# Performance work log

Hardware: AMD Instinct MI355X
Metric: run time of the kernel (lower is better)

## Reference

```python
import jax, jax.numpy as jnp
import numpy as np

NUM_LAYERS = 4
HIDDEN = 64
IN_CH = 3
OUT_CH = 1


def setup_inputs() -> dict:
    key = jax.random.key(0)
    ks = jax.random.split(key, 16)
    s = 0.1  # weight init scale
    x = jax.random.normal(ks[0], (2, 64, 64, IN_CH), dtype=jnp.float32)
    lift_w = jax.random.normal(ks[1], (IN_CH, HIDDEN), dtype=jnp.float32) * s
    lift_b = jax.random.normal(ks[2], (HIDDEN,), dtype=jnp.float32) * s
    blk_w = jax.random.normal(ks[3], (NUM_LAYERS, HIDDEN, HIDDEN), dtype=jnp.float32) * s
    blk_b = jax.random.normal(ks[4], (NUM_LAYERS, HIDDEN), dtype=jnp.float32) * s
    q_w = jax.random.normal(ks[5], (NUM_LAYERS, HIDDEN, HIDDEN), dtype=jnp.float32) * s
    q_b = jax.random.normal(ks[6], (NUM_LAYERS, HIDDEN), dtype=jnp.float32) * s
    k_w = jax.random.normal(ks[7], (NUM_LAYERS, HIDDEN, HIDDEN), dtype=jnp.float32) * s
    k_b = jax.random.normal(ks[8], (NUM_LAYERS, HIDDEN), dtype=jnp.float32) * s
    v_w = jax.random.normal(ks[9], (NUM_LAYERS, HIDDEN, HIDDEN), dtype=jnp.float32) * s
    v_b = jax.random.normal(ks[10], (NUM_LAYERS, HIDDEN), dtype=jnp.float32) * s
    proj_w = jax.random.normal(ks[11], (HIDDEN, OUT_CH), dtype=jnp.float32) * s
    proj_b = jax.random.normal(ks[12], (OUT_CH,), dtype=jnp.float32) * s
    return {"x": x, "lift_w": lift_w, "lift_b": lift_b,
            "blk_w": blk_w, "blk_b": blk_b,
            "q_w": q_w, "q_b": q_b, "k_w": k_w, "k_b": k_b,
            "v_w": v_w, "v_b": v_b, "proj_w": proj_w, "proj_b": proj_b}


def reference(x, lift_w, lift_b, blk_w, blk_b, q_w, q_b, k_w, k_b, v_w, v_b, proj_w, proj_b):
    prefix = x.shape[:-1]           # (B, H, W)
    B = x.shape[0]
    xf = x.reshape(B, -1, x.shape[-1])   # [B, N, in_ch]
    N = xf.shape[1]
    h = xf @ lift_w + lift_b             # [B, N, d]
    d = h.shape[-1]
    scale = 1.0 / jnp.sqrt(jnp.float32(d))
    for i in range(NUM_LAYERS):
        q = h @ q_w[i] + q_b[i]
        k = h @ k_w[i] + k_b[i]
        v = h @ v_w[i] + v_b[i]
        # full dense kernel, as in torch.bmm(q, k^T)/sqrt(d)
        kern = jnp.einsum('bnd,bmd->bnm', q, k) * scale     # [B, N, N]
        integral = jnp.einsum('bnm,bmd->bnd', kern, v) / N  # [B, N, d]
        wh = h @ blk_w[i] + blk_b[i]
        h = jax.nn.gelu(wh + integral, approximate=False)   # torch F.gelu default = exact erf
    out = h @ proj_w + proj_b                               # [B, N, out_ch]
    return out.reshape(*prefix, out.shape[-1])
```

## Files before the change

kernel.cpp:

```cpp
#include <hip/hip_runtime.h>
#include <hip/hip_bf16.h>
#include <math.h>


#define NLAYER 4
#define NB 2
#define NN 4096
#define DD 64
#define RPB 32
#define NT 256
#define NBLK 256
#define SHP 68
#define C0F (1.0f/32768.0f)
#define PSZ 2304
#define NCH 128
#define CHW 18

typedef __hip_bfloat16 bf16;
typedef unsigned long long u64t;

__device__ __forceinline__ float b2f(const bf16 v) { return __bfloat162float(v); }

template <typename T> struct Acc;
template <> struct Acc<float> {
    static __device__ __forceinline__ float ld(const void* p, int i) { return ((const float*)p)[i]; }
    static __device__ __forceinline__ void st(void* p, int i, float v) { ((float*)p)[i] = v; }
};
template <> struct Acc<bf16> {
    static __device__ __forceinline__ float ld(const void* p, int i) { return b2f(((const bf16*)p)[i]); }
    static __device__ __forceinline__ void st(void* p, int i, float v) { ((bf16*)p)[i] = __float2bfloat16(v); }
};

__device__ __forceinline__ float gelu_exact(float x) {
    return 0.5f * x * (1.0f + erff(x * 0.70710678118654752f));
}

__device__ __forceinline__ float2 ldc2(const float* p) {
    u64t v = __hip_atomic_load((const u64t*)p, __ATOMIC_RELAXED, __HIP_MEMORY_SCOPE_AGENT);
    float2 r;
    r.x = __uint_as_float((unsigned)v);
    r.y = __uint_as_float((unsigned)(v >> 32));
    return r;
}
__device__ __forceinline__ void stc2(float* p, float a, float b) {
    u64t v = ((u64t)__float_as_uint(b) << 32) | (u64t)__float_as_uint(a);
    __hip_atomic_store((u64t*)p, v, __ATOMIC_RELAXED, __HIP_MEMORY_SCOPE_AGENT);
}
__device__ __forceinline__ unsigned ldw(unsigned* p) {
    return __hip_atomic_load(p, __ATOMIC_RELAXED, __HIP_MEMORY_SCOPE_AGENT);
}
__device__ __forceinline__ void stw(unsigned* p, unsigned v) {
    __hip_atomic_store(p, v, __ATOMIC_RELAXED, __HIP_MEMORY_SCOPE_AGENT);
}
__device__ __forceinline__ void pollw(unsigned* p, unsigned ep) {
    int guard = 0;
    while (ldw(p) < ep && ++guard < (1 << 18)) __builtin_amdgcn_s_sleep(2);
}

__device__ __forceinline__ void mm4x4(float (&acc)[4][4],
    float4 L0, float4 L1, float4 L2, float4 L3,
    float4 R0, float4 R1, float4 R2, float4 R3)
{
    const float L[4][4] = {{L0.x,L0.y,L0.z,L0.w},{L1.x,L1.y,L1.z,L1.w},
                           {L2.x,L2.y,L2.z,L2.w},{L3.x,L3.y,L3.z,L3.w}};
    const float R[4][4] = {{R0.x,R0.y,R0.z,R0.w},{R1.x,R1.y,R1.z,R1.w},
                           {R2.x,R2.y,R2.z,R2.w},{R3.x,R3.y,R3.z,R3.w}};
    #pragma unroll
    for (int a = 0; a < 4; a++)
        #pragma unroll
        for (int k = 0; k < 4; k++)
            #pragma unroll
            for (int b = 0; b < 4; b++)
                acc[a][b] += L[a][k] * R[k][b];
}

__device__ __forceinline__ void mmNT4x4(float (&acc)[4][4],
    float4 L0, float4 L1, float4 L2, float4 L3,
    float4 R0, float4 R1, float4 R2, float4 R3)
{
    const float L[4][4] = {{L0.x,L0.y,L0.z,L0.w},{L1.x,L1.y,L1.z,L1.w},
                           {L2.x,L2.y,L2.z,L2.w},{L3.x,L3.y,L3.z,L3.w}};
    const float R[4][4] = {{R0.x,R0.y,R0.z,R0.w},{R1.x,R1.y,R1.z,R1.w},
                           {R2.x,R2.y,R2.z,R2.w},{R3.x,R3.y,R3.z,R3.w}};
    #pragma unroll
    for (int a = 0; a < 4; a++)
        #pragma unroll
        for (int b = 0; b < 4; b++)
            #pragma unroll
            for (int k = 0; k < 4; k++)
                acc[a][b] += L[a][k] * R[b][k];
}

__device__ __forceinline__ void outer4x4(float (&acc)[4][4], float4 A, float4 B)
{
    const float Aa[4] = {A.x, A.y, A.z, A.w};
    const float Ba[4] = {B.x, B.y, B.z, B.w};
    #pragma unroll
    for (int a = 0; a < 4; a++)
        #pragma unroll
        for (int b = 0; b < 4; b++)
            acc[a][b] += Aa[a] * Ba[b];
}


#define SM_SS   23936
#define SM_SU   24000
#define SM_BK   24064
#define SM_BQ   24128
#define SM_BV   24192
#define SM_BE   24256
#define SM_QK   24320
#define SM_KQ   24384
#define SM_QBK  24448
#define SM_RED  24512
#define SM_TOT  24768

template <typename T>
__device__ void run_net(
    const void* x, const void* lw, const void* lb,
    const void* blkw, const void* blkb,
    const void* qw, const void* qb, const void* kw, const void* kb,
    const void* vw, const void* vb, const void* pw, const void* pb,
    void* out, float* Gpart, float* Gg,
    unsigned* aflag, unsigned* cflag,
    float* smem, int blk, int t)
{
    float (*sH)[SHP] = (float(*)[SHP])(smem);
    float (*B1)[SHP] = (float(*)[SHP])(smem + 2176);
    float (*B2)[SHP] = (float(*)[SHP])(smem + 6528);
    float (*B3)[SHP] = (float(*)[SHP])(smem + 10880);
    float (*B4)[SHP] = (float(*)[SHP])(smem + 15232);
    float (*B5)[SHP] = (float(*)[SHP])(smem + 19584);
    float* PS  = smem + 10880;
    float* RED = smem + 10880;
    float* sS  = smem + SM_SS;
    float* suS = smem + SM_SU;
    float* bkS = smem + SM_BK;
    float* bqS = smem + SM_BQ;
    float* bvS = smem + SM_BV;
    float* beS = smem + SM_BE;
    float* qkS = smem + SM_QK;
    float* kqS = smem + SM_KQ;
    float* qbkS = smem + SM_QBK;
    float (*red)[DD] = (float(*)[DD])(smem + SM_RED);

    const int row0 = blk * RPB;
    const int bb = blk >> 7;
    const int r = t >> 4, c4 = (t & 15) << 2;
    const int i4 = t >> 4, j4 = t & 15;
    const int r0 = i4 << 2, c0 = j4 << 2;

    #pragma unroll
    for (int a = 0; a < 2; a++) {
        const int row = r + 16 * a, gr = row0 + row;
        float x0 = Acc<T>::ld(x, gr * 3 + 0);
        float x1 = Acc<T>::ld(x, gr * 3 + 1);
        float x2 = Acc<T>::ld(x, gr * 3 + 2);
        float o[4];
        #pragma unroll
        for (int b = 0; b < 4; b++) {
            int c = c4 + b;
            o[b] = Acc<T>::ld(lb, c) + x0 * Acc<T>::ld(lw, c)
                 + x1 * Acc<T>::ld(lw, DD + c) + x2 * Acc<T>::ld(lw, 2 * DD + c);
        }
        *(float4*)&sH[row][c4] = make_float4(o[0], o[1], o[2], o[3]);
    }
    __syncthreads();

    for (int layer = 0; layer < NLAYER; layer++) {
        const unsigned ep = (unsigned)(layer + 1);
        float* GgL = Gg + (size_t)(layer * NB + bb) * PSZ;
        const int wOff = layer * DD * DD, bOff = layer * DD;

        {
            if (i4 <= j4) {
                float m[4][4];
                #pragma unroll
                for (int a = 0; a < 4; a++)
                    #pragma unroll
                    for (int b = 0; b < 4; b++) m[a][b] = 0.f;
                #pragma unroll 8
                for (int n = 0; n < RPB; n++)
                    outer4x4(m, *(const float4*)&sH[n][r0], *(const float4*)&sH[n][c0]);
                float* dst = PS + (i4 * (33 - i4) / 2 + (j4 - i4)) * 16;
                #pragma unroll
                for (int a = 0; a < 4; a++)
                    #pragma unroll
                    for (int b = 0; b < 4; b++) dst[a * 4 + b] = m[a][b];
            }
            if (t < DD) {
                float ss = 0.f;
                #pragma unroll 8
                for (int n = 0; n < RPB; n++) ss += sH[n][t];
                PS[2176 + t] = ss;
                PS[2240 + t] = 0.f;
            }
        }
        __syncthreads();
        {
            float* slot = Gpart + (size_t)blk * PSZ;
            #pragma unroll
            for (int k2 = 0; k2 < 4; k2++) {
                const int idx = 2 * (t + k2 * NT);
                stc2(&slot[idx], PS[idx], PS[idx + 1]);
            }
            if (t < 128) {
                const int idx = 2 * (t + 4 * NT);
                stc2(&slot[idx], PS[idx], PS[idx + 1]);
            }
        }
        __syncthreads();
        if (t == 0) stw(&aflag[blk], ep);

        for (int i2 = t; i2 < DD * DD; i2 += NT) {
            B1[i2 >> 6][i2 & 63] = Acc<T>::ld(qw, wOff + i2);
            B4[i2 >> 6][i2 & 63] = Acc<T>::ld(kw, wOff + i2);
        }
        if (t < DD) {
            bkS[t] = Acc<T>::ld(kb, bOff + t);
            bqS[t] = Acc<T>::ld(qb, bOff + t);
            bvS[t] = Acc<T>::ld(vb, bOff + t);
        }

        {
            if (t < NCH) pollw(&aflag[bb * NCH + t], ep);
            __syncthreads();
            const int chunk = blk & (NCH - 1);
            if (t < 144) {
                const int g = t / 9, p2 = t % 9;
                const float* base = Gpart + (size_t)(bb * NCH + g * 8) * PSZ
                                  + chunk * CHW + 2 * p2;
                float ax = 0.f, ay = 0.f;
                #pragma unroll
                for (int s2 = 0; s2 < 8; s2++) {
                    float2 v = ldc2(base + (size_t)s2 * PSZ);
                    ax += v.x; ay += v.y;
                }
                RED[g * 20 + 2 * p2]     = ax;
                RED[g * 20 + 2 * p2 + 1] = ay;
            }
            __syncthreads();
            if (t < 9) {
                float s0 = 0.f, s1 = 0.f;
                #pragma unroll
                for (int g = 0; g < 16; g++) {
                    s0 += RED[g * 20 + 2 * t];
                    s1 += RED[g * 20 + 2 * t + 1];
                }
                stc2(&GgL[chunk * CHW + 2 * t], s0, s1);
            }
            __syncthreads();
            if (t == 0) stw(&cflag[blk], ep);
        }

        {
            float acc[4][4];
            #pragma unroll
            for (int a = 0; a < 4; a++)
                #pragma unroll
                for (int b = 0; b < 4; b++) acc[a][b] = 0.f;
            #pragma unroll 2
            for (int e = 0; e < DD; e += 4)
                mmNT4x4(acc,
                      *(const float4*)&B1[r0 + 0][e], *(const float4*)&B1[r0 + 1][e],
                      *(const float4*)&B1[r0 + 2][e], *(const float4*)&B1[r0 + 3][e],
                      *(const float4*)&B4[c0 + 0][e], *(const float4*)&B4[c0 + 1][e],
                      *(const float4*)&B4[c0 + 2][e], *(const float4*)&B4[c0 + 3][e]);
            #pragma unroll
            for (int a = 0; a < 4; a++)
                *(float4*)&B2[r0 + a][c0] = make_float4(acc[a][0], acc[a][1], acc[a][2], acc[a][3]);

            if (t < DD) {
                float u = 0.f;
                for (int e = 0; e < DD; e++) u += B1[t][e] * bkS[e];
                qkS[t] = u;
            } else if (t < 2 * DD) {
                const int rr = t - DD;
                float u = 0.f;
                for (int e = 0; e < DD; e++) u += B4[rr][e] * bqS[e];
                kqS[rr] = u;
            } else if (t == 2 * DD) {
                float u = 0.f;
                for (int e = 0; e < DD; e++) u += bqS[e] * bkS[e];
                qbkS[0] = u;
            }
        }
        __syncthreads();
        for (int i2 = t; i2 < DD * DD; i2 += NT) {
            B1[i2 >> 6][i2 & 63] = Acc<T>::ld(vw, wOff + i2);
            B4[i2 >> 6][i2 & 63] = Acc<T>::ld(blkw, wOff + i2);
        }

        {
            if (t < NCH) pollw(&cflag[bb * NCH + t], ep);
            __syncthreads();
            if (i4 <= j4) {
                const float* src = GgL + (i4 * (33 - i4) / 2 + (j4 - i4)) * 16;
                #pragma unroll
                for (int a = 0; a < 4; a++)
                    *(float4*)&B3[r0 + a][c0] = *(const float4*)&src[a * 4];
            } else {
                const float* src = GgL + (j4 * (33 - j4) / 2 + (i4 - j4)) * 16;
                #pragma unroll
                for (int a = 0; a < 4; a++)
                    #pragma unroll
                    for (int b = 0; b < 4; b++)
                        B3[r0 + a][c0 + b] = src[b * 4 + a];
            }
            if (t < DD) sS[t] = GgL[2176 + t];
            __syncthreads();
        }

        {
            float acc[4][4];
            #pragma unroll
            for (int a = 0; a < 4; a++)
                #pragma unroll
                for (int b = 0; b < 4; b++) acc[a][b] = sS[r0 + a] * bvS[c0 + b];
            #pragma unroll 2
            for (int e = 0; e < DD; e += 4)
                mm4x4(acc,
                      *(const float4*)&B3[r0 + 0][e], *(const float4*)&B3[r0 + 1][e],
                      *(const float4*)&B3[r0 + 2][e], *(const float4*)&B3[r0 + 3][e],
                      *(const float4*)&B1[e + 0][c0], *(const float4*)&B1[e + 1][c0],
                      *(const float4*)&B1[e + 2][c0], *(const float4*)&B1[e + 3][c0]);
            #pragma unroll
            for (int a = 0; a < 4; a++)
                *(float4*)&B5[r0 + a][c0] = make_float4(acc[a][0], acc[a][1], acc[a][2], acc[a][3]);
        }
        {
            const int c = t & 63, q = t >> 6;
            float u = 0.f;
            #pragma unroll
            for (int d2 = 0; d2 < 16; d2++) u += sS[q * 16 + d2] * B1[q * 16 + d2][c];
            red[q][c] = u;
        }
        __syncthreads();
        if (t < DD) suS[t] = red[0][t] + red[1][t] + red[2][t] + red[3][t] + (float)NN * bvS[t];
        __syncthreads();

        {
            float acc[4][4];
            #pragma unroll
            for (int a = 0; a < 4; a++)
                #pragma unroll
                for (int b = 0; b < 4; b++) acc[a][b] = qkS[r0 + a] * suS[c0 + b];
            #pragma unroll 2
            for (int e = 0; e < DD; e += 4)
                mm4x4(acc,
                      *(const float4*)&B2[r0 + 0][e], *(const float4*)&B2[r0 + 1][e],
                      *(const float4*)&B2[r0 + 2][e], *(const float4*)&B2[r0 + 3][e],
                      *(const float4*)&B5[e + 0][c0], *(const float4*)&B5[e + 1][c0],
                      *(const float4*)&B5[e + 2][c0], *(const float4*)&B5[e + 3][c0]);
            float wloc[4][4];
            #pragma unroll
            for (int a = 0; a < 4; a++)
                #pragma unroll
                for (int b = 0; b < 4; b++)
                    wloc[a][b] = B4[r0 + a][c0 + b] + C0F * acc[a][b];
            {
                const int c = t & 63, q = t >> 6;
                float u = 0.f;
                #pragma unroll
                for (int e2 = 0; e2 < 16; e2++) u += kqS[q * 16 + e2] * B5[q * 16 + e2][c];
                red[q][c] = u;
            }
            __syncthreads();
            #pragma unroll
            for (int a = 0; a < 4; a++)
                *(float4*)&B3[r0 + a][c0] = make_float4(wloc[a][0], wloc[a][1], wloc[a][2], wloc[a][3]);
            if (t < DD) beS[t] = Acc<T>::ld(blkb, bOff + t)
                               + C0F * (red[0][t] + red[1][t] + red[2][t] + red[3][t]
                                        + qbkS[0] * suS[t]);
        }
        __syncthreads();

        float o[2][4];
        #pragma unroll
        for (int a = 0; a < 2; a++) {
            const int row = r + 16 * a;
            float acc2[4];
            #pragma unroll
            for (int b = 0; b < 4; b++) acc2[b] = beS[c4 + b];
            for (int d = 0; d < DD; d++) {
                float hv = sH[row][d];
                float4 w4 = *(const float4*)&B3[d][c4];
                acc2[0] += hv * w4.x; acc2[1] += hv * w4.y;
                acc2[2] += hv * w4.z; acc2[3] += hv * w4.w;
            }
            #pragma unroll
            for (int b = 0; b < 4; b++) o[a][b] = gelu_exact(acc2[b]);
        }

        if (layer == NLAYER - 1) {
            float pbv = Acc<T>::ld(pb, 0);
            #pragma unroll
            for (int a = 0; a < 2; a++) {
                float p = 0.f;
                #pragma unroll
                for (int b = 0; b < 4; b++) p += o[a][b] * Acc<T>::ld(pw, c4 + b);
                p += __shfl_xor(p, 1);
                p += __shfl_xor(p, 2);
                p += __shfl_xor(p, 4);
                p += __shfl_xor(p, 8);
                if ((t & 15) == 0) Acc<T>::st(out, row0 + r + 16 * a, p + pbv);
            }
        } else {
            __syncthreads();
            #pragma unroll
            for (int a = 0; a < 2; a++)
                *(float4*)&sH[r + 16 * a][c4] =
                    make_float4(o[a][0], o[a][1], o[a][2], o[a][3]);
            __syncthreads();
        }
    }
}

__global__ __launch_bounds__(NT) void gno_kernel(
    const void* x, const void* lw, const void* lb,
    const void* blkw, const void* blkb,
    const void* qw, const void* qb, const void* kw, const void* kb,
    const void* vw, const void* vb, const void* pw, const void* pb,
    void* out, float* Gpart, float* Gg, unsigned* bar, int mode)
{
    __shared__ alignas(16) float smem[SM_TOT];
    __shared__ int stot;

    const int blk = blockIdx.x, t = threadIdx.x;

    bool isbf;
    if (mode >= 0) {
        isbf = (mode == 1);
    } else {
        if (t == 0) stot = 0;
        __syncthreads();
        int cdt = 0;
        const unsigned int* xw = (const unsigned int*)x;
        for (int i = t; i < 8192; i += NT) {
            unsigned u = xw[i] & 0xFFFFu;
            int e = (u >> 7) & 0xFF;
            cdt += (u == 0u || (e >= 100 && e <= 142)) ? 1 : 0;
        }
        atomicAdd(&stot, cdt);
        __syncthreads();
        isbf = (stot > 4915);
    }

    unsigned* aflag = bar;
    unsigned* cflag = bar + 256;

    if (isbf)
        run_net<bf16>(x, lw, lb, blkw, blkb, qw, qb, kw, kb, vw, vb, pw, pb,
                      out, Gpart, Gg, aflag, cflag, smem, blk, t);
    else
        run_net<float>(x, lw, lb, blkw, blkb, qw, qb, kw, kb, vw, vb, pw, pb,
                       out, Gpart, Gg, aflag, cflag, smem, blk, t);
}

extern "C" void kernel_launch(void* const* d_in, const int* in_sizes, int n_in,
                              void* d_out, int out_size, void* d_ws, size_t ws_size,
                              hipStream_t stream)
{
    const void* x    = d_in[0];
    const void* lw   = d_in[1];
    const void* lb   = d_in[2];
    const void* blkw = d_in[3];
    const void* blkb = d_in[4];
    const void* qw   = d_in[5];
    const void* qb   = d_in[6];
    const void* kw   = d_in[7];
    const void* kb   = d_in[8];
    const void* vw   = d_in[9];
    const void* vb   = d_in[10];
    const void* pw   = d_in[11];
    const void* pb   = d_in[12];

    int mode = -1;
    if (in_sizes && n_in > 0) {
        if (in_sizes[0] == 49152) mode = 1;
        else if (in_sizes[0] == 98304) mode = 0;
    }

    unsigned* bar = (unsigned*)d_ws;
    float* Gpart  = (float*)d_ws + 512;
    float* Gg     = Gpart + (size_t)NBLK * PSZ;

    hipMemsetAsync(bar, 0, 512 * sizeof(unsigned), stream);
    gno_kernel<<<NBLK, NT, 0, stream>>>(x, lw, lb, blkw, blkb, qw, qb, kw, kb,
                                        vw, vb, pw, pb, d_out, Gpart, Gg, bar, mode);
}
```

Measured before the change: 159.4 us.

## Prefetch layer weights via direct-to-LDS loads and move QK^T product before grid barrier

Weight matrices for q/k and v/blk are now fetched with global_load_lds DMA (fp32) or register-staged packed loads (bf16), issued early so their latency overlaps the Gram partial computation and the cross-block wait. The Wq·Wk^T product and the bias projections are computed before the grid-wide barrier instead of after it, using an explicit LDS transpose of Wk and unpadded 64-wide weight buffers. This takes per-layer weight setup off the critical path after the barrier, at the cost of extra syncthreads, possible LDS bank conflicts from the unpadded layout, and more registers for staging.

```diff
diff --git a/kernel.cpp b/kernel.cpp
--- a/kernel.cpp
+++ b/kernel.cpp
@@ -19,7 +19,28 @@
 typedef __hip_bfloat16 bf16;
 typedef unsigned long long u64t;
 
+#define O_SH   0
+#define O_B3   2176
+#define O_W1   6528
+#define O_W2   10624
+#define O_W4   14720
+#define O_W5   18816
+#define O_SS   22912
+#define O_SU   22976
+#define O_BK   23040
+#define O_BQ   23104
+#define O_BV   23168
+#define O_BE   23232
+#define O_QK   23296
+#define O_KQ   23360
+#define O_QBK  23424
+#define O_RED  23488
+#define SM_TOT 23744
+
 __device__ __forceinline__ float b2f(const bf16 v) { return __bfloat162float(v); }
+__device__ __forceinline__ float bfu(unsigned s) {
+    return __uint_as_float(s << 16);
+}
 
 template <typename T> struct Acc;
 template <> struct Acc<float> {
@@ -33,6 +54,12 @@
 
 __device__ __forceinline__ float gelu_exact(float x) {
     return 0.5f * x * (1.0f + erff(x * 0.70710678118654752f));
+}
+
+__device__ __forceinline__ void dma16(const float* g, float* l) {
+    __builtin_amdgcn_global_load_lds(
+        (const __attribute__((address_space(1))) unsigned int*)g,
+        (__attribute__((address_space(3))) unsigned int*)l, 16, 0, 0);
 }
 
 __device__ __forceinline__ float2 ldc2(const float* p) {
@@ -74,23 +101,6 @@
                 acc[a][b] += L[a][k] * R[k][b];
 }
 
-__device__ __forceinline__ void mmNT4x4(float (&acc)[4][4],
-    float4 L0, float4 L1, float4 L2, float4 L3,
-    float4 R0, float4 R1, float4 R2, float4 R3)
-{
-    const float L[4][4] = {{L0.x,L0.y,L0.z,L0.w},{L1.x,L1.y,L1.z,L1.w},
-                           {L2.x,L2.y,L2.z,L2.w},{L3.x,L3.y,L3.z,L3.w}};
-    const float R[4][4] = {{R0.x,R0.y,R0.z,R0.w},{R1.x,R1.y,R1.z,R1.w},
-                           {R2.x,R2.y,R2.z,R2.w},{R3.x,R3.y,R3.z,R3.w}};
-    #pragma unroll
-    for (int a = 0; a < 4; a++)
-        #pragma unroll
-        for (int b = 0; b < 4; b++)
-            #pragma unroll
-            for (int k = 0; k < 4; k++)
-                acc[a][b] += L[a][k] * R[b][k];
-}
-
 __device__ __forceinline__ void outer4x4(float (&acc)[4][4], float4 A, float4 B)
 {
     const float Aa[4] = {A.x, A.y, A.z, A.w};
@@ -101,19 +111,6 @@
         for (int b = 0; b < 4; b++)
             acc[a][b] += Aa[a] * Ba[b];
 }
-
-
-#define SM_SS   23936
-#define SM_SU   24000
-#define SM_BK   24064
-#define SM_BQ   24128
-#define SM_BV   24192
-#define SM_BE   24256
-#define SM_QK   24320
-#define SM_KQ   24384
-#define SM_QBK  24448
-#define SM_RED  24512
-#define SM_TOT  24768
 
 template <typename T>
 __device__ void run_net(
@@ -125,30 +122,33 @@
     unsigned* aflag, unsigned* cflag,
     float* smem, int blk, int t)
 {
-    float (*sH)[SHP] = (float(*)[SHP])(smem);
-    float (*B1)[SHP] = (float(*)[SHP])(smem + 2176);
-    float (*B2)[SHP] = (float(*)[SHP])(smem + 6528);
-    float (*B3)[SHP] = (float(*)[SHP])(smem + 10880);
-    float (*B4)[SHP] = (float(*)[SHP])(smem + 15232);
-    float (*B5)[SHP] = (float(*)[SHP])(smem + 19584);
-    float* PS  = smem + 10880;
-    float* RED = smem + 10880;
-    float* sS  = smem + SM_SS;
-    float* suS = smem + SM_SU;
-    float* bkS = smem + SM_BK;
-    float* bqS = smem + SM_BQ;
-    float* bvS = smem + SM_BV;
-    float* beS = smem + SM_BE;
-    float* qkS = smem + SM_QK;
-    float* kqS = smem + SM_KQ;
-    float* qbkS = smem + SM_QBK;
-    float (*red)[DD] = (float(*)[DD])(smem + SM_RED);
+    float (*sH)[SHP] = (float(*)[SHP])(smem + O_SH);
+    float (*B3)[SHP] = (float(*)[SHP])(smem + O_B3);
+    float (*W1)[DD]  = (float(*)[DD])(smem + O_W1);
+    float (*W2)[DD]  = (float(*)[DD])(smem + O_W2);
+    float (*W4)[DD]  = (float(*)[DD])(smem + O_W4);
+    float (*W5)[DD]  = (float(*)[DD])(smem + O_W5);
+    float* W1f = smem + O_W1;
+    float* W4f = smem + O_W4;
+    float* PS  = smem + O_B3;
+    float* RED = smem + O_B3;
+    float* sS  = smem + O_SS;
+    float* suS = smem + O_SU;
+    float* bkS = smem + O_BK;
+    float* bqS = smem + O_BQ;
+    float* bvS = smem + O_BV;
+    float* beS = smem + O_BE;
+    float* qkS = smem + O_QK;
+    float* kqS = smem + O_KQ;
+    float* qbkS = smem + O_QBK;
+    float (*red)[DD] = (float(*)[DD])(smem + O_RED);
 
     const int row0 = blk * RPB;
     const int bb = blk >> 7;
     const int r = t >> 4, c4 = (t & 15) << 2;
     const int i4 = t >> 4, j4 = t & 15;
     const int r0 = i4 << 2, c0 = j4 << 2;
+    const int Ltr = t & 63, gtr = t >> 6;
 
     #pragma unroll
     for (int a = 0; a < 2; a++) {
@@ -167,10 +167,30 @@
     }
     __syncthreads();
 
+    unsigned pq[8], pk[8];
+
     for (int layer = 0; layer < NLAYER; layer++) {
         const unsigned ep = (unsigned)(layer + 1);
         float* GgL = Gg + (size_t)(layer * NB + bb) * PSZ;
         const int wOff = layer * DD * DD, bOff = layer * DD;
+
+        if constexpr (sizeof(T) == 4) {
+            const float* qwf = (const float*)qw + wOff;
+            const float* kwf = (const float*)kw + wOff;
+            #pragma unroll
+            for (int k = 0; k < 4; k++) {
+                dma16(qwf + 4 * (k * NT + t), &W1f[4 * (k * NT + t)]);
+                dma16(kwf + 4 * (k * NT + t), &W4f[4 * (k * NT + t)]);
+            }
+        } else {
+            const unsigned* q32 = (const unsigned*)qw + (wOff >> 1);
+            const unsigned* k32 = (const unsigned*)kw + (wOff >> 1);
+            #pragma unroll
+            for (int k = 0; k < 8; k++) {
+                pq[k] = q32[t + k * NT];
+                pk[k] = k32[t + k * NT];
+            }
+        }
 
         {
             if (i4 <= j4) {
@@ -212,14 +232,79 @@
         __syncthreads();
         if (t == 0) stw(&aflag[blk], ep);
 
-        for (int i2 = t; i2 < DD * DD; i2 += NT) {
-            B1[i2 >> 6][i2 & 63] = Acc<T>::ld(qw, wOff + i2);
-            B4[i2 >> 6][i2 & 63] = Acc<T>::ld(kw, wOff + i2);
-        }
         if (t < DD) {
             bkS[t] = Acc<T>::ld(kb, bOff + t);
             bqS[t] = Acc<T>::ld(qb, bOff + t);
             bvS[t] = Acc<T>::ld(vb, bOff + t);
+        }
+        if constexpr (sizeof(T) != 4) {
+            #pragma unroll
+            for (int k = 0; k < 8; k++) {
+                const int i2 = t + k * NT;
+                unsigned uq = pq[k], uk = pk[k];
+                *(float2*)&W1f[2 * i2] = make_float2(bfu(uq & 0xffffu), bfu(uq >> 16));
+                *(float2*)&W4f[2 * i2] = make_float2(bfu(uk & 0xffffu), bfu(uk >> 16));
+            }
+        }
+        __syncthreads();
+
+        #pragma unroll
+        for (int k = 0; k < 16; k++) {
+            const int i = (Ltr + gtr + 4 * k) & 63;
+            W5[i][Ltr] = W4[Ltr][i];
+        }
+        __syncthreads();
+
+        {
+            float acc[4][4];
+            #pragma unroll
+            for (int a = 0; a < 4; a++)
+                #pragma unroll
+                for (int b = 0; b < 4; b++) acc[a][b] = 0.f;
+            #pragma unroll 2
+            for (int e = 0; e < DD; e += 4)
+                mm4x4(acc,
+                      *(const float4*)&W1[r0 + 0][e], *(const float4*)&W1[r0 + 1][e],
+                      *(const float4*)&W1[r0 + 2][e], *(const float4*)&W1[r0 + 3][e],
+                      *(const float4*)&W5[e + 0][c0], *(const float4*)&W5[e + 1][c0],
+                      *(const float4*)&W5[e + 2][c0], *(const float4*)&W5[e + 3][c0]);
+            #pragma unroll
+            for (int a = 0; a < 4; a++)
+                *(float4*)&W2[r0 + a][c0] = make_float4(acc[a][0], acc[a][1], acc[a][2], acc[a][3]);
+
+            if (t < DD) {
+                float u = 0.f;
+                for (int e = 0; e < DD; e++) u += W1[t][e] * bkS[e];
+                qkS[t] = u;
+            } else if (t < 2 * DD) {
+                const int rr = t - DD;
+                float u = 0.f;
+                for (int e = 0; e < DD; e++) u += W4[rr][e] * bqS[e];
+                kqS[rr] = u;
+            } else if (t == 2 * DD) {
+                float u = 0.f;
+                for (int e = 0; e < DD; e++) u += bqS[e] * bkS[e];
+                qbkS[0] = u;
+            }
+        }
+        __syncthreads();
+
+        if constexpr (sizeof(T) == 4) {
+            const float* vwf = (const float*)vw + wOff;
+            const float* bwf = (const float*)blkw + wOff;
+            #pragma unroll
+            for (int k = 0; k < 4; k++) {
+                dma16(vwf + 4 * (k * NT + t), &W1f[4 * (k * NT + t)]);
+                dma16(bwf + 4 * (k * NT + t), &W4f[4 * (k * NT + t)]);
+            }
+        } else {
+            const unsigned* v32 = (const unsigned*)vw + (wOff >> 1);
+            const unsigned* b32 = (const unsigned*)blkw + (wOff >> 1);
+            #pragma unroll
+            for (int k = 0; k < 8; k++) {
+                pq[k] = v32[t + k * NT];
+                pk[k] = b32[t + k * NT];
+            }
         }
 
         {
@@ -253,42 +338,14 @@
             if (t == 0) stw(&cflag[blk], ep);
         }
 
-        {
-            float acc[4][4];
-            #pragma unroll
-            for (int a = 0; a < 4; a++)
-                #pragma unroll
-                for (int b = 0; b < 4; b++) acc[a][b] = 0.f;
-            #pragma unroll 2
-            for (int e = 0; e < DD; e += 4)
-                mmNT4x4(acc,
-                      *(const float4*)&B1[r0 + 0][e], *(const float4*)&B1[r0 + 1][e],
-                      *(const float4*)&B1[r0 + 2][e], *(const float4*)&B1[r0 + 3][e],
-                      *(const float4*)&B4[c0 + 0][e], *(const float4*)&B4[c0 + 1][e],
-                      *(const float4*)&B4[c0 + 2][e], *(const float4*)&B4[c0 + 3][e]);
-            #pragma unroll
-            for (int a = 0; a < 4; a++)
-                *(float4*)&B2[r0 + a][c0] = make_float4(acc[a][0], acc[a][1], acc[a][2], acc[a][3]);
-
-            if (t < DD) {
-                float u = 0.f;
-                for (int e = 0; e < DD; e++) u += B1[t][e] * bkS[e];
-                qkS[t] = u;
-            } else if (t < 2 * DD) {
-                const int rr = t - DD;
-                float u = 0.f;
-                for (int e = 0; e < DD; e++) u += B4[rr][e] * bqS[e];
-                kqS[rr] = u;
-            } else if (t == 2 * DD) {
-                float u = 0.f;
-                for (int e = 0; e < DD; e++) u += bqS[e] * bkS[e];
-                qbkS[0] = u;
-            }
-        }
-        __syncthreads();
-        for (int i2 = t; i2 < DD * DD; i2 += NT) {
-            B1[i2 >> 6][i2 & 63] = Acc<T>::ld(vw, wOff + i2);
-            B4[i2 >> 6][i2 & 63] = Acc<T>::ld(blkw, wOff + i2);
+        if constexpr (sizeof(T) != 4) {
+            #pragma unroll
+            for (int k = 0; k < 8; k++) {
+                const int i2 = t + k * NT;
+                unsigned uv = pq[k], ub = pk[k];
+                *(float2*)&W1f[2 * i2] = make_float2(bfu(uv & 0xffffu), bfu(uv >> 16));
+                *(float2*)&W4f[2 * i2] = make_float2(bfu(ub & 0xffffu), bfu(ub >> 16));
+            }
         }
 
         {
@@ -322,17 +379,17 @@
                 mm4x4(acc,
                       *(const float4*)&B3[r0 + 0][e], *(const float4*)&B3[r0 + 1][e],
                       *(const float4*)&B3[r0 + 2][e], *(const float4*)&B3[r0 + 3][e],
-                      *(const float4*)&B1[e + 0][c0], *(const float4*)&B1[e + 1][c0],
-                      *(const float4*)&B1[e + 2][c0], *(const float4*)&B1[e + 3][c0]);
-            #pragma unroll
-            for (int a = 0; a < 4; a++)
-                *(float4*)&B5[r0 + a][c0] = make_float4(acc[a][0], acc[a][1], acc[a][2], acc[a][3]);
+                      *(const float4*)&W1[e + 0][c0], *(const float4*)&W1[e + 1][c0],
+                      *(const float4*)&W1[e + 2][c0], *(const float4*)&W1[e + 3][c0]);
+            #pragma unroll
+            for (int a = 0; a < 4; a++)
+                *(float4*)&W5[r0 + a][c0] = make_float4(acc[a][0], acc[a][1], acc[a][2], acc[a][3]);
         }
         {
             const int c = t & 63, q = t >> 6;
             float u = 0.f;
             #pragma unroll
-            for (int d2 = 0; d2 < 16; d2++) u += sS[q * 16 + d2] * B1[q * 16 + d2][c];
+            for (int d2 = 0; d2 < 16; d2++) u += sS[q * 16 + d2] * W1[q * 16 + d2][c];
             red[q][c] = u;
         }
         __syncthreads();
@@ -348,21 +405,21 @@
             #pragma unroll 2
             for (int e = 0; e < DD; e += 4)
                 mm4x4(acc,
-                      *(const float4*)&B2[r0 + 0][e], *(const float4*)&B2[r0 + 1][e],
-                      *(const float4*)&B2[r0 + 2][e], *(const float4*)&B2[r0 + 3][e],
-                      *(const float4*)&B5[e + 0][c0], *(const float4*)&B5[e + 1][c0],
-                      *(const float4*)&B5[e + 2][c0], *(const float4*)&B5[e + 3][c0]);
+                      *(const float4*)&W2[r0 + 0][e], *(const float4*)&W2[r0 + 1][e],
+                      *(const float4*)&W2[r0 + 2][e], *(const float4*)&W2[r0 + 3][e],
+                      *(const float4*)&W5[e + 0][c0], *(const float4*)&W5[e + 1][c0],
+                      *(const float4*)&W5[e + 2][c0], *(const float4*)&W5[e + 3][c0]);
             float wloc[4][4];
             #pragma unroll
             for (int a = 0; a < 4; a++)
                 #pragma unroll
                 for (int b = 0; b < 4; b++)
-                    wloc[a][b] = B4[r0 + a][c0 + b] + C0F * acc[a][b];
+                    wloc[a][b] = W4[r0 + a][c0 + b] + C0F * acc[a][b];
             {
                 const int c = t & 63, q = t >> 6;
                 float u = 0.f;
                 #pragma unroll
-                for (int e2 = 0; e2 < 16; e2++) u += kqS[q * 16 + e2] * B5[q * 16 + e2][c];
+                for (int e2 = 0; e2 < 16; e2++) u += kqS[q * 16 + e2] * W5[q * 16 + e2][c];
                 red[q][c] = u;
             }
             __syncthreads();
@@ -416,7 +473,7 @@
     }
 }
 
-__global__ __launch_bounds__(NT) void gno_kernel(
+__global__ __launch_bounds__(NT, 1) void gno_kernel(
     const void* x, const void* lw, const void* lb,
     const void* blkw, const void* blkb,
     const void* qw, const void* qb, const void* kw, const void* kb,
```

New measurement: 173.5 us. +8.9%, slower.
